# Kernel optimization log

Measured on AMD Instinct MI355X. Metric: run time of the kernel, lower is better.

Reference implementation:

```python
import jax, jax.numpy as jnp
import numpy as np

N = 100000   # nodes
E = 300000   # edges (avg degree ~3, molecular graphs)
DIN = 128    # input node features
H = 512      # hidden
OUT = 256    # out_channels
G = 4096     # number of graphs
EPS = 1e-5
SLOPE = 0.01  # LeakyReLU default negative slope
SELF_W = 2.0  # improved=True self-loop weight


def setup_inputs() -> dict:
    key = jax.random.key(0)
    ks = jax.random.split(key, 12)
    x = jax.random.normal(ks[0], (N, DIN), dtype=jnp.float32)
    edge_index = jax.random.randint(ks[1], (2, E), 0, N, dtype=jnp.int64)
    batch = jnp.sort(jax.random.randint(ks[2], (N,), 0, G, dtype=jnp.int64))
    s1 = 1.0 / np.sqrt(DIN)
    s2 = 1.0 / np.sqrt(H)
    return {
        "x": x,
        "edge_index": edge_index,
        "batch": batch,
        "W1": jax.random.normal(ks[3], (DIN, H), dtype=jnp.float32) * s1,
        "b1": jax.random.normal(ks[4], (H,), dtype=jnp.float32) * 0.01,
        "g1": jax.random.uniform(ks[5], (H,), dtype=jnp.float32, minval=0.5, maxval=1.5),
        "beta1": jax.random.normal(ks[6], (H,), dtype=jnp.float32) * 0.01,
        "W2": jax.random.normal(ks[7], (H, H), dtype=jnp.float32) * s2,
        "b2": jax.random.normal(ks[8], (H,), dtype=jnp.float32) * 0.01,
        "g2": jax.random.uniform(ks[9], (H,), dtype=jnp.float32, minval=0.5, maxval=1.5),
        "beta2": jax.random.normal(ks[10], (H,), dtype=jnp.float32) * 0.01,
        "Wf": jax.random.normal(ks[11], (H, OUT), dtype=jnp.float32) * s2,
        "bf": jnp.zeros((OUT,), dtype=jnp.float32),
    }


def _gcn_conv(x, W, b, row, col, n):
    # GCNConv(improved=True, add_self_loops=True, normalize=True), edge_weight=None
    h = x @ W                                   # [n, H]
    ones = jnp.ones(row.shape[0], dtype=h.dtype)
    deg = jax.ops.segment_sum(ones, col, num_segments=n) + SELF_W
    dinv = jax.lax.rsqrt(deg)                   # deg > 0 always (self-loop weight 2)
    norm = dinv[row] * dinv[col]                # [E]
    agg = jax.ops.segment_sum(h[row] * norm[:, None], col, num_segments=n)
    agg = agg + h * (SELF_W * dinv * dinv)[:, None]  # self-loop messages, no edge materialization
    return agg + b


def _bn(x, g, beta):
    # training-mode BatchNorm1d: biased batch stats
    mu = jnp.mean(x, axis=0)
    var = jnp.mean(jnp.square(x - mu), axis=0)
    return g * (x - mu) * jax.lax.rsqrt(var + EPS) + beta


def reference(x, edge_index, batch, W1, b1, g1, beta1, W2, b2, g2, beta2, Wf, bf):
    row, col = edge_index[0], edge_index[1]
    n = x.shape[0]
    h = _gcn_conv(x, W1, b1, row, col, n)
    h = jax.nn.leaky_relu(_bn(h, g1, beta1), SLOPE)
    # dropout is identity in eval mode
    h = _gcn_conv(h, W2, b2, row, col, n)
    h = jax.nn.leaky_relu(_bn(h, g2, beta2), SLOPE)
    pooled = jax.ops.segment_max(h, batch, num_segments=G)
    pooled = jnp.where(jnp.isfinite(pooled), pooled, 0.0)  # empty graphs -> 0 (torch_scatter fill)
    return pooled @ Wf + bf
```

## Files before the change

kernel.cpp:

```cpp
#include <hip/hip_runtime.h>
#include <hip/hip_bf16.h>

typedef __hip_bfloat16 bf16;
typedef __attribute__((ext_vector_type(8))) short short8;
typedef __attribute__((ext_vector_type(4))) float f32x4;

#define HDIM 512
#define SLOPE 0.01f
#define BN_EPS 1e-5f
#define STRIPES 8

__device__ inline float bf2f(short s) {
    unsigned u = ((unsigned)(unsigned short)s) << 16;
    return __builtin_bit_cast(float, u);
}
__device__ inline unsigned short f2bfbits(float v) {
    bf16 h = __float2bfloat16(v);
    return (unsigned short)__builtin_bit_cast(short, h);
}

struct EdgeRec { int src; float nm; };

__global__ void detect_types(const int* __restrict__ ei, const unsigned* __restrict__ xw,
                             int* __restrict__ flags, float* __restrict__ gpart) {
    __shared__ int nzhi, okbf;
    if (threadIdx.x == 0) { nzhi = 0; okbf = 0; }
    __syncthreads();
    int lo = 0, ok = 0;
    for (int i = threadIdx.x; i < 2048; i += 256)
        if (ei[2 * i + 1] != 0) lo++;
    for (int i = threadIdx.x; i < 1024; i += 256) {
        unsigned w = (xw[i] & 0xFFFFu) << 16;
        float av = fabsf(__builtin_bit_cast(float, w));
        if (av > 0.0009f && av < 64.0f) ok++;
    }
    for (int i = threadIdx.x; i < STRIPES * 2 * HDIM; i += 256) gpart[i] = 0.f;
    if (lo) atomicAdd(&nzhi, lo);
    if (ok) atomicAdd(&okbf, ok);
    __syncthreads();
    if (threadIdx.x == 0) {
        flags[0] = (nzhi == 0) ? 1 : 0;
        flags[1] = (okbf < 512) ? 1 : 0;
    }
}

__global__ void conv_all_idx(const int* __restrict__ ei, const int* __restrict__ batch,
                             int* __restrict__ ei32, int* __restrict__ batch32,
                             int* __restrict__ cnt, int e2, int n,
                             const int* __restrict__ flags) {
    int i = blockIdx.x * blockDim.x + threadIdx.x;
    int i64 = flags[0];
    if (i < e2) {
        int v = i64 ? (int)((const long long*)ei)[i] : ei[i];
        ei32[i] = v;
        if (i >= e2 / 2) atomicAdd(&cnt[v], 1);
    } else if (i < e2 + n) {
        int j = i - e2;
        batch32[j] = i64 ? (int)((const long long*)batch)[j] : batch[j];
    }
}

__global__ void wt_conv_all(const void* __restrict__ W1, const void* __restrict__ W2,
                            const void* __restrict__ Wf, const void* __restrict__ bf_,
                            bf16* __restrict__ W1T, bf16* __restrict__ W2T,
                            bf16* __restrict__ WfT, bf16* __restrict__ bfbf,
                            const int* __restrict__ flags) {
    const int S1 = 128 * 512, S2 = 512 * 512, S3 = 512 * 256;
    int idx = blockIdx.x * 256 + threadIdx.x;
    bool f32 = flags[1] != 0;
    if (idx < S1) {
        int nn = idx / 128, k = idx - nn * 128;
        float v = f32 ? ((const float*)W1)[(size_t)k * 512 + nn]
                      : __bfloat162float(((const bf16*)W1)[(size_t)k * 512 + nn]);
        W1T[idx] = __float2bfloat16(v);
    } else if (idx < S1 + S2) {
        int t = idx - S1;
        int nn = t / 512, k = t - nn * 512;
        float v = f32 ? ((const float*)W2)[(size_t)k * 512 + nn]
                      : __bfloat162float(((const bf16*)W2)[(size_t)k * 512 + nn]);
        W2T[t] = __float2bfloat16(v);
    } else if (idx < S1 + S2 + S3) {
        int t = idx - S1 - S2;
        int nn = t / 512, k = t - nn * 512;
        float v = f32 ? ((const float*)Wf)[(size_t)k * 256 + nn]
                      : __bfloat162float(((const bf16*)Wf)[(size_t)k * 256 + nn]);
        WfT[t] = __float2bfloat16(v);
    } else if (idx < S1 + S2 + S3 + 256) {
        int t = idx - S1 - S2 - S3;
        float v = f32 ? ((const float*)bf_)[t]
                      : __bfloat162float(((const bf16*)bf_)[t]);
        bfbf[t] = __float2bfloat16(v);
    }
}

__global__ void finalize_deg(const int* __restrict__ cnt, float* __restrict__ dinv,
                             float* __restrict__ selfw, int n) {
    int i = blockIdx.x * blockDim.x + threadIdx.x;
    if (i < n) {
        float d = (float)cnt[i] + 2.0f;
        dinv[i] = rsqrtf(d);
        selfw[i] = 2.0f / d;
    }
}

__global__ __launch_bounds__(256) void scan_part(
    const int* __restrict__ counts, int* __restrict__ offsets,
    int* __restrict__ bsum, int n)
{
    __shared__ int s[512];
    int b = blockIdx.x;
    int base = b * 512;
    int t = threadIdx.x;
    s[t]       = (base + t       < n) ? counts[base + t]       : 0;
    s[t + 256] = (base + t + 256 < n) ? counts[base + t + 256] : 0;

    int offset = 1;
    for (int d = 256; d > 0; d >>= 1) {
        __syncthreads();
        if (t < d) {
            int ai = offset * (2 * t + 1) - 1;
            int bi = offset * (2 * t + 2) - 1;
            s[bi] += s[ai];
        }
        offset <<= 1;
    }
    __syncthreads();
    if (t == 0) { bsum[b] = s[511]; s[511] = 0; }
    for (int d = 1; d < 512; d <<= 1) {
        offset >>= 1;
        __syncthreads();
        if (t < d) {
            int ai = offset * (2 * t + 1) - 1;
            int bi = offset * (2 * t + 2) - 1;
            int tmp = s[ai]; s[ai] = s[bi]; s[bi] += tmp;
        }
    }
    __syncthreads();
    if (base + t < n)       offsets[base + t]       = s[t];
    if (base + t + 256 < n) offsets[base + t + 256] = s[t + 256];
}

__global__ __launch_bounds__(1024) void scan_tops(int* __restrict__ bsum, int nb) {
    __shared__ int s[1024];
    int t = threadIdx.x;
    s[t] = (t < nb) ? bsum[t] : 0;
    __syncthreads();
    for (int off = 1; off < 1024; off <<= 1) {
        int v = (t >= off) ? s[t - off] : 0;
        __syncthreads();
        s[t] += v;
        __syncthreads();
    }
    if (t < nb) bsum[t] = (t == 0) ? 0 : s[t - 1];
}

__global__ __launch_bounds__(256) void scan_add(
    int* __restrict__ offsets, const int* __restrict__ bsum, int n, int e)
{
    int b = blockIdx.x;
    int base = b * 512;
    int add = bsum[b];
    int t = threadIdx.x;
    if (base + t < n)       offsets[base + t]       += add;
    if (base + t + 256 < n) offsets[base + t + 256] += add;
    if (b == 0 && t == 0) offsets[n] = e;
}

__global__ void scatter_edges(const int* __restrict__ rows, const int* __restrict__ cols,
                              const int* __restrict__ offsets, int* __restrict__ cursor,
                              const float* __restrict__ dinv,
                              EdgeRec* __restrict__ er, int e)
{
    int i = blockIdx.x * blockDim.x + threadIdx.x;
    if (i < e) {
        int d = cols[i];
        int r = rows[i];
        int pos = offsets[d] + atomicAdd(&cursor[d], 1);
        EdgeRec rec;
        rec.src = r;
        rec.nm = dinv[d] * dinv[r];
        er[pos] = rec;
    }
}

#define GEMM_STAGE(boff, kk)                                                             \
    {                                                                                    \
        _Pragma("unroll")                                                                \
        for (int i_ = 0; i_ < 2; i_++) {                                                 \
            int c_ = wave * 2 + i_;                                                      \
            const bf16* ga_ = A  + (size_t)(m0 + c_ * 16 + lrow) * K + (kk) + lcol;      \
            const bf16* gb_ = BT + (size_t)(n0 + c_ * 16 + lrow) * K + (kk) + lcol;      \
            __builtin_amdgcn_global_load_lds(                                            \
                (const __attribute__((address_space(1))) unsigned*)ga_,                  \
                (__attribute__((address_space(3))) unsigned*)(smem + (boff) + c_ * 512), \
                16, 0, 0);                                                               \
            __builtin_amdgcn_global_load_lds(                                            \
                (const __attribute__((address_space(1))) unsigned*)gb_,                  \
                (__attribute__((address_space(3))) unsigned*)(smem + 8192 + (boff) + c_ * 512), \
                16, 0, 0);                                                               \
        }                                                                                \
    }

#define GEMM_COMPUTE(boff)                                                               \
    {                                                                                    \
        short8 a[4], b[4];                                                               \
        _Pragma("unroll")                                                                \
        for (int mi2 = 0; mi2 < 4; mi2++)                                                \
            a[mi2] = *(const short8*)&smem[(boff) + (wm + mi2 * 16 + r) * 32 + aoff];    \
        _Pragma("unroll")                                                                \
        for (int ni = 0; ni < 4; ni++)                                                   \
            b[ni] = *(const short8*)&smem[8192 + (boff) + (wn + ni * 16 + r) * 32 + aoff]; \
        _Pragma("unroll")                                                                \
        for (int mi2 = 0; mi2 < 4; mi2++)                                                \
            _Pragma("unroll")                                                            \
            for (int ni = 0; ni < 4; ni++)                                               \
                acc[mi2][ni] = __builtin_amdgcn_mfma_f32_16x16x32_bf16(                  \
                    a[mi2], b[ni], acc[mi2][ni], 0, 0, 0);                               \
    }

template<bool STATS>
__global__ __launch_bounds__(256, 4) void gemm_m97(
    const bf16* __restrict__ A, const bf16* __restrict__ BT,
    void* __restrict__ C, const bf16* __restrict__ bias,
    int M, int K, int N, const int* __restrict__ cf32,
    float* __restrict__ gpart, int MB)
{
    __shared__ bf16 smem[16384];

    int NBN = N >> 7;
    int id = blockIdx.x;
    int grp = id / (8 * NBN);
    int loc = id - grp * 8 * NBN;
    int mi = loc & 7;
    int nblk = loc >> 3;
    int mblk = grp * 8 + mi;
    if (mblk >= MB) return;

    int tid = threadIdx.x;
    int wave = tid >> 6, lane = tid & 63, q = lane >> 4, r = lane & 15;
    int wm = (wave >> 1) * 64, wn = (wave & 1) * 64;
    int m0 = mblk * 128, n0 = nblk * 128;
    bool c32 = cf32 && *cf32;

    int lrow = lane >> 2;
    int lcol = (((lane & 3) ^ ((lane >> 3) & 3)) * 8);
    int aoff = (q ^ ((r >> 1) & 3)) * 8;

    f32x4 acc[4][4];
#pragma unroll
    for (int mi2 = 0; mi2 < 4; mi2++)
#pragma unroll
        for (int ni = 0; ni < 4; ni++)
            acc[mi2][ni] = {0.f, 0.f, 0.f, 0.f};

    const int nK = K >> 5;

    GEMM_STAGE(0, 0);
    __syncthreads();

    int cur = 0;
    for (int t = 1; t < nK; ++t) {
        GEMM_STAGE(cur ^ 4096, t * 32);
        GEMM_COMPUTE(cur);
        __syncthreads();
        cur ^= 4096;
    }
    GEMM_COMPUTE(cur);

    if (!c32) {
        __syncthreads();
#pragma unroll
        for (int mi2 = 0; mi2 < 4; mi2++) {
#pragma unroll
            for (int ni = 0; ni < 4; ni++) {
                int lc = wn + ni * 16 + r;
                float bv = bias ? __bfloat162float(bias[n0 + lc]) : 0.f;
#pragma unroll
                for (int reg = 0; reg < 4; reg++) {
                    int lr = wm + mi2 * 16 + q * 4 + reg;
                    int bo = ((lr << 8) + (lc << 1)) ^ (q << 5);
                    *(bf16*)((char*)smem + bo) = __float2bfloat16(acc[mi2][ni][reg] + bv);
                }
            }
        }
        __syncthreads();
#pragma unroll
        for (int pss = 0; pss < 8; pss++) {
            int off = pss * 4096 + tid * 16;
            int row = off >> 8;
            int cb = off & 255;
            int rb = cb ^ (((row >> 2) & 3) << 5);
            f32x4 v = *(const f32x4*)((const char*)smem + (row << 8) + rb);
            int gm = m0 + row;
            if (gm < M)
                *(f32x4*)((char*)C + (((size_t)gm * N + n0) << 1) + cb) = v;
        }
    } else {
#pragma unroll
        for (int mi2 = 0; mi2 < 4; mi2++) {
#pragma unroll
            for (int ni = 0; ni < 4; ni++) {
                int gn = n0 + wn + ni * 16 + r;
                float bv = bias ? __bfloat162float(bias[gn]) : 0.f;
#pragma unroll
                for (int reg = 0; reg < 4; reg++) {
                    int gm = m0 + wm + mi2 * 16 + q * 4 + reg;
                    if (gm < M)
                        ((float*)C)[(size_t)gm * N + gn] = acc[mi2][ni][reg] + bv;
                }
            }
        }
    }

    if constexpr (STATS) {
        float* base = gpart + (size_t)(mblk & (STRIPES - 1)) * 2 * HDIM;
#pragma unroll
        for (int ni = 0; ni < 4; ni++) {
            float cs = 0.f, cq = 0.f;
#pragma unroll
            for (int mi2 = 0; mi2 < 4; mi2++)
#pragma unroll
                for (int reg = 0; reg < 4; reg++) {
                    int gm = m0 + wm + mi2 * 16 + q * 4 + reg;
                    if (gm < M) {
                        float v = acc[mi2][ni][reg];
                        cs += v; cq += v * v;
                    }
                }
            cs += __shfl_xor(cs, 16, 64);
            cs += __shfl_xor(cs, 32, 64);
            cq += __shfl_xor(cq, 16, 64);
            cq += __shfl_xor(cq, 32, 64);
            if (q == 0) {
                int c = n0 + wn + ni * 16 + r;
                atomicAdd(&base[c], cs);
                atomicAdd(&base[HDIM + c], cq);
            }
        }
    }
}

__global__ __launch_bounds__(256) void agg_csr_din(
    const void* __restrict__ x, const int* __restrict__ offsets,
    const EdgeRec* __restrict__ er, const float* __restrict__ selfw,
    bf16* __restrict__ out, int n, const int* __restrict__ flags)
{
    int wave = threadIdx.x >> 6, lane = threadIdx.x & 63;
    int gw = blockIdx.x * 4 + wave;
    int nw = gridDim.x * 4;
    bool f32 = flags[1] != 0;

    for (int dst = gw; dst < n; dst += nw) {
        int s0 = offsets[dst], s1 = offsets[dst + 1];
        float sw = selfw[dst];
        float a0, a1;
        if (f32) {
            float2 v = ((const float2*)x)[(size_t)dst * 64 + lane];
            a0 = sw * v.x; a1 = sw * v.y;
        } else {
            unsigned u = ((const unsigned*)x)[(size_t)dst * 64 + lane];
            a0 = sw * bf2f((short)(u & 0xFFFF)); a1 = sw * bf2f((short)(u >> 16));
        }
        int p = s0;
        for (; p + 1 < s1; p += 2) {
            EdgeRec e0 = er[p], e1 = er[p + 1];
            if (f32) {
                float2 v0 = ((const float2*)x)[(size_t)e0.src * 64 + lane];
                float2 v1 = ((const float2*)x)[(size_t)e1.src * 64 + lane];
                a0 += e0.nm * v0.x + e1.nm * v1.x;
                a1 += e0.nm * v0.y + e1.nm * v1.y;
            } else {
                unsigned u0 = ((const unsigned*)x)[(size_t)e0.src * 64 + lane];
                unsigned u1 = ((const unsigned*)x)[(size_t)e1.src * 64 + lane];
                a0 += e0.nm * bf2f((short)(u0 & 0xFFFF)) + e1.nm * bf2f((short)(u1 & 0xFFFF));
                a1 += e0.nm * bf2f((short)(u0 >> 16))    + e1.nm * bf2f((short)(u1 >> 16));
            }
        }
        if (p < s1) {
            EdgeRec e0 = er[p];
            if (f32) {
                float2 v0 = ((const float2*)x)[(size_t)e0.src * 64 + lane];
                a0 += e0.nm * v0.x; a1 += e0.nm * v0.y;
            } else {
                unsigned u0 = ((const unsigned*)x)[(size_t)e0.src * 64 + lane];
                a0 += e0.nm * bf2f((short)(u0 & 0xFFFF)); a1 += e0.nm * bf2f((short)(u0 >> 16));
            }
        }
        ((unsigned*)out)[(size_t)dst * 64 + lane] =
            (unsigned)f2bfbits(a0) | ((unsigned)f2bfbits(a1) << 16);
    }
}

__global__ __launch_bounds__(256) void agg_csr_bn(
    const bf16* __restrict__ h, const int* __restrict__ offsets,
    const EdgeRec* __restrict__ er, const float* __restrict__ selfw,
    const float* __restrict__ scale, const float* __restrict__ shift,
    bf16* __restrict__ y, int n)
{
    int wave = threadIdx.x >> 6, lane = threadIdx.x & 63;
    int f0 = lane * 8;
    int gw = blockIdx.x * 4 + wave;
    int nw = gridDim.x * 4;

    float sc[8], sh[8];
#pragma unroll
    for (int j = 0; j < 8; j++) { sc[j] = scale[f0 + j]; sh[j] = shift[f0 + j]; }

    for (int dst = gw; dst < n; dst += nw) {
        int s0 = offsets[dst], s1 = offsets[dst + 1];
        float sw = selfw[dst];
        short8 hv = *(const short8*)(h + (size_t)dst * HDIM + f0);
        float acc[8];
#pragma unroll
        for (int j = 0; j < 8; j++) {
            float t = sc[j] * bf2f(hv[j]) + sh[j];
            t = t > 0.f ? t : SLOPE * t;
            acc[j] = sw * t;
        }
        int p = s0;
        for (; p + 1 < s1; p += 2) {
            EdgeRec e0 = er[p], e1 = er[p + 1];
            short8 v0 = *(const short8*)(h + (size_t)e0.src * HDIM + f0);
            short8 v1 = *(const short8*)(h + (size_t)e1.src * HDIM + f0);
#pragma unroll
            for (int j = 0; j < 8; j++) {
                float t0 = sc[j] * bf2f(v0[j]) + sh[j];
                t0 = t0 > 0.f ? t0 : SLOPE * t0;
                float t1 = sc[j] * bf2f(v1[j]) + sh[j];
                t1 = t1 > 0.f ? t1 : SLOPE * t1;
                acc[j] += e0.nm * t0 + e1.nm * t1;
            }
        }
        if (p < s1) {
            EdgeRec e0 = er[p];
            short8 v0 = *(const short8*)(h + (size_t)e0.src * HDIM + f0);
#pragma unroll
            for (int j = 0; j < 8; j++) {
                float t0 = sc[j] * bf2f(v0[j]) + sh[j];
                t0 = t0 > 0.f ? t0 : SLOPE * t0;
                acc[j] += e0.nm * t0;
            }
        }
        short8 o;
#pragma unroll
        for (int j = 0; j < 8; j++) ((bf16*)&o)[j] = __float2bfloat16(acc[j]);
        *(short8*)(y + (size_t)dst * HDIM + f0) = o;
    }
}

__global__ void bn_final(float* __restrict__ gpart,
                         const void* __restrict__ gamma, const void* __restrict__ beta,
                         float* __restrict__ scale, float* __restrict__ shift,
                         float invN, const int* __restrict__ flags)
{
    int f = threadIdx.x;
    float s = 0.f, q = 0.f;
#pragma unroll
    for (int k = 0; k < STRIPES; k++) {
        s += gpart[(size_t)k * 2 * HDIM + f];
        q += gpart[(size_t)k * 2 * HDIM + HDIM + f];
        gpart[(size_t)k * 2 * HDIM + f] = 0.f;
        gpart[(size_t)k * 2 * HDIM + HDIM + f] = 0.f;
    }
    float g = flags[1] ? ((const float*)gamma)[f]
                       : __bfloat162float(((const bf16*)gamma)[f]);
    float b = flags[1] ? ((const float*)beta)[f]
                       : __bfloat162float(((const bf16*)beta)[f]);
    float mu = s * invN;
    float var = fmaxf(q * invN - mu * mu, 0.f);
    float inv = rsqrtf(var + BN_EPS);
    float sc = g * inv;
    scale[f] = sc;
    shift[f] = b - mu * sc;
}

__global__ __launch_bounds__(256) void pool_fused(
    const bf16* __restrict__ y, const int* __restrict__ batch,
    const float* __restrict__ scale, const float* __restrict__ shift,
    bf16* __restrict__ pooled, int n, int G)
{
    int wave = threadIdx.x >> 6, lane = threadIdx.x & 63;
    int g = blockIdx.x * 4 + wave;
    if (g >= G) return;
    int f0 = lane * 8;

    int lo = 0, hi = n;
    while (lo < hi) { int mid = (lo + hi) >> 1; if (batch[mid] < g) lo = mid + 1; else hi = mid; }
    int s = lo;
    hi = n;
    while (lo < hi) { int mid = (lo + hi) >> 1; if (batch[mid] <= g) lo = mid + 1; else hi = mid; }
    int e = lo;

    float mx[8], mn[8];
#pragma unroll
    for (int j = 0; j < 8; j++) { mx[j] = -3.0e38f; mn[j] = 3.0e38f; }

    int rr = s;
    for (; rr + 1 < e; rr += 2) {
        short8 v0 = *(const short8*)(y + (size_t)rr * HDIM + f0);
        short8 v1 = *(const short8*)(y + (size_t)(rr + 1) * HDIM + f0);
#pragma unroll
        for (int j = 0; j < 8; j++) {
            float a = bf2f(v0[j]), b = bf2f(v1[j]);
            mx[j] = fmaxf(mx[j], fmaxf(a, b));
            mn[j] = fminf(mn[j], fminf(a, b));
        }
    }
    if (rr < e) {
        short8 v0 = *(const short8*)(y + (size_t)rr * HDIM + f0);
#pragma unroll
        for (int j = 0; j < 8; j++) {
            float a = bf2f(v0[j]);
            mx[j] = fmaxf(mx[j], a);
            mn[j] = fminf(mn[j], a);
        }
    }

    short8 o;
#pragma unroll
    for (int j = 0; j < 8; j++) {
        float outv = 0.f;
        if (s < e) {
            float sc = scale[f0 + j];
            float t = sc * (sc >= 0.f ? mx[j] : mn[j]) + shift[f0 + j];
            outv = t > 0.f ? t : SLOPE * t;
        }
        ((bf16*)&o)[j] = __float2bfloat16(outv);
    }
    *(short8*)(pooled + (size_t)g * HDIM + f0) = o;
}

extern "C" void kernel_launch(void* const* d_in, const int* in_sizes, int n_in,
                              void* d_out, int out_size, void* d_ws, size_t ws_size,
                              hipStream_t stream)
{
    const void* x     = d_in[0];
    const int*  ei    = (const int*)d_in[1];
    const int*  batch = (const int*)d_in[2];

    const int N   = in_sizes[2];
    const int E   = in_sizes[1] / 2;
    const int DIN = 128;
    const int OUT = 256;
    const int G   = out_size / OUT;
    const int Mp  = (N + 127) & ~127;
    const int MB  = Mp / 128;
    const int MB8 = (MB + 7) & ~7;

    char* p = (char*)d_ws;
    bf16* B1     = (bf16*)p;  p += (size_t)Mp * HDIM * sizeof(bf16);
    bf16* B2     = (bf16*)p;  p += (size_t)Mp * HDIM * sizeof(bf16);
    bf16* Q      = (bf16*)p;  p += (size_t)Mp * DIN * sizeof(bf16);
    bf16* W1T    = (bf16*)p;  p += (size_t)HDIM * DIN * sizeof(bf16);
    bf16* W2T    = (bf16*)p;  p += (size_t)HDIM * HDIM * sizeof(bf16);
    bf16* WfT    = (bf16*)p;  p += (size_t)OUT * HDIM * sizeof(bf16);
    bf16* bfbf   = (bf16*)p;  p += 512 * sizeof(bf16);
    int* ei32    = (int*)p;   p += (size_t)2 * E * sizeof(int);
    int* batch32 = (int*)p;   p += (size_t)N * sizeof(int);
    float* dinv  = (float*)p; p += (size_t)N * sizeof(float);
    float* selfw = (float*)p; p += (size_t)N * sizeof(float);
    int* offsets = (int*)p;   p += (size_t)(N + 4) * sizeof(int);
    int* cursor  = (int*)p;   p += (size_t)N * sizeof(int);
    EdgeRec* er  = (EdgeRec*)p; p += (size_t)E * sizeof(EdgeRec);
    int* bsum    = (int*)p;   p += 1024 * sizeof(int);
    float* gpart = (float*)p; p += (size_t)STRIPES * 2 * HDIM * sizeof(float);
    float* sc1   = (float*)p; p += HDIM * sizeof(float);
    float* sh1   = (float*)p; p += HDIM * sizeof(float);
    float* sc2   = (float*)p; p += HDIM * sizeof(float);
    float* sh2   = (float*)p; p += HDIM * sizeof(float);
    int* flags   = (int*)p;   p += 4 * sizeof(int);

    detect_types<<<1, 256, 0, stream>>>(ei, (const unsigned*)x, flags, gpart);
    hipMemsetAsync(cursor, 0, (size_t)N * sizeof(int), stream);
    conv_all_idx<<<(2 * E + N + 255) / 256, 256, 0, stream>>>(
        ei, batch, ei32, batch32, cursor, 2 * E, N, flags);
    wt_conv_all<<<(128 * 512 + 512 * 512 + 512 * 256 + 256 + 255) / 256, 256, 0, stream>>>(
        d_in[3], d_in[7], d_in[11], d_in[12], W1T, W2T, WfT, bfbf, flags);

    const int* rows = ei32;
    const int* cols = ei32 + E;

    finalize_deg<<<(N + 255) / 256, 256, 0, stream>>>(cursor, dinv, selfw, N);
    int nb = (N + 511) / 512;
    scan_part<<<nb, 256, 0, stream>>>(cursor, offsets, bsum, N);
    scan_tops<<<1, 1024, 0, stream>>>(bsum, nb);
    scan_add<<<nb, 256, 0, stream>>>(offsets, bsum, N, E);
    hipMemsetAsync(cursor, 0, (size_t)N * sizeof(int), stream);
    scatter_edges<<<(E + 255) / 256, 256, 0, stream>>>(rows, cols, offsets, cursor,
                                                       dinv, er, E);

    int gemm_blocks = MB8 * (HDIM / 128);

    agg_csr_din<<<2048, 256, 0, stream>>>(x, offsets, er, selfw, Q, N, flags);
    gemm_m97<true><<<gemm_blocks, 256, 0, stream>>>(
        Q, W1T, B2, nullptr, N, DIN, HDIM, nullptr, gpart, MB);
    bn_final<<<1, HDIM, 0, stream>>>(gpart, d_in[5], d_in[6], sc1, sh1, 1.0f / N, flags);

    agg_csr_bn<<<2048, 256, 0, stream>>>(B2, offsets, er, selfw, sc1, sh1, B1, N);
    gemm_m97<true><<<gemm_blocks, 256, 0, stream>>>(
        B1, W2T, B2, nullptr, N, HDIM, HDIM, nullptr, gpart, MB);
    bn_final<<<1, HDIM, 0, stream>>>(gpart, d_in[9], d_in[10], sc2, sh2, 1.0f / N, flags);

    pool_fused<<<(G + 3) / 4, 256, 0, stream>>>(B2, batch32, sc2, sh2, Q, N, G);
    gemm_m97<false><<<(G / 128) * (OUT / 128), 256, 0, stream>>>(
        Q, WfT, d_out, bfbf, G, HDIM, OUT, flags + 1, nullptr, G / 128);
}
```

Measured before the change: 460.9 us.

## Prefetch next node and unroll edge gathers by four in CSR aggregation

Both CSR aggregation kernels now software-pipeline across destination nodes: the offsets, self weight and self row for the next node are loaded before the current node's edges are processed. The edge loop is unrolled to four gathers per iteration, and the tail is handled without a loop, so more independent memory loads are in flight to hide gather latency. The GEMM launch bounds also move from 4 to 5 waves per SIMD, which caps registers to allow higher occupancy. The cost is higher register pressure in the aggregation kernels and possible spills in the GEMM.

```diff
diff --git a/kernel.cpp b/kernel.cpp
--- a/kernel.cpp
+++ b/kernel.cpp
@@ -219,7 +219,7 @@
     }
 
 template<bool STATS>
-__global__ __launch_bounds__(256, 4) void gemm_m97(
+__global__ __launch_bounds__(256, 5) void gemm_m97(
     const bf16* __restrict__ A, const bf16* __restrict__ BT,
     void* __restrict__ C, const bf16* __restrict__ bias,
     int M, int K, int N, const int* __restrict__ cf32,
@@ -340,6 +340,53 @@
     }
 }
 
+#define AGG_DIN_BODY(LOADV)                                                            \
+    int dst = gw;                                                                      \
+    if (dst < n) {                                                                     \
+        int s0 = offsets[dst], s1 = offsets[dst + 1];                                  \
+        float sw = selfw[dst];                                                         \
+        float h0, h1; LOADV(dst, h0, h1);                                              \
+        while (dst < n) {                                                              \
+            int nd = dst + nw;                                                         \
+            int ns0 = 0, ns1 = 0; float nsw = 0.f, nh0 = 0.f, nh1 = 0.f;               \
+            if (nd < n) {                                                              \
+                ns0 = offsets[nd]; ns1 = offsets[nd + 1]; nsw = selfw[nd];             \
+                LOADV(nd, nh0, nh1);                                                   \
+            }                                                                          \
+            float a0 = sw * h0, a1 = sw * h1;                                          \
+            int p = s0;                                                                \
+            for (; p + 3 < s1; p += 4) {                                               \
+                EdgeRec e0 = er[p], e1 = er[p + 1], e2 = er[p + 2], e3 = er[p + 3];    \
+                float x0, y0, x1, y1, x2, y2, x3, y3;                                  \
+                LOADV(e0.src, x0, y0); LOADV(e1.src, x1, y1);                          \
+                LOADV(e2.src, x2, y2); LOADV(e3.src, x3, y3);                          \
+                a0 += e0.nm * x0 + e1.nm * x1 + e2.nm * x2 + e3.nm * x3;               \
+                a1 += e0.nm * y0 + e1.nm * y1 + e2.nm * y2 + e3.nm * y3;               \
+            }                                                                          \
+            int rem = s1 - p;                                                          \
+            if (rem > 0) {                                                             \
+                EdgeRec e0 = er[p], e1 = e0, e2 = e0;                                  \
+                if (rem > 1) e1 = er[p + 1];                                           \
+                if (rem > 2) e2 = er[p + 2];                                           \
+                float x0, y0, x1 = 0.f, y1 = 0.f, x2 = 0.f, y2 = 0.f;                  \
+                LOADV(e0.src, x0, y0);                                                 \
+                if (rem > 1) LOADV(e1.src, x1, y1);                                    \
+                if (rem > 2) LOADV(e2.src, x2, y2);                                    \
+                a0 += e0.nm * x0; a1 += e0.nm * y0;                                    \
+                if (rem > 1) { a0 += e1.nm * x1; a1 += e1.nm * y1; }                   \
+                if (rem > 2) { a0 += e2.nm * x2; a1 += e2.nm * y2; }                   \
+            }                                                                          \
+            ((unsigned*)out)[(size_t)dst * 64 + lane] =                                \
+                (unsigned)f2bfbits(a0) | ((unsigned)f2bfbits(a1) << 16);               \
+            dst = nd; s0 = ns0; s1 = ns1; sw = nsw; h0 = nh0; h1 = nh1;                \
+        }                                                                              \
+    }
+
+#define LOADF32(idx, a, b) { float2 v_ = ((const float2*)x)[(size_t)(idx) * 64 + lane]; \
+                             a = v_.x; b = v_.y; }
+#define LOADBF(idx, a, b)  { unsigned u_ = ((const unsigned*)x)[(size_t)(idx) * 64 + lane]; \
+                             a = bf2f((short)(u_ & 0xFFFF)); b = bf2f((short)(u_ >> 16)); }
+
 __global__ __launch_bounds__(256) void agg_csr_din(
     const void* __restrict__ x, const int* __restrict__ offsets,
     const EdgeRec* __restrict__ er, const float* __restrict__ selfw,
@@ -349,45 +396,15 @@
     int gw = blockIdx.x * 4 + wave;
     int nw = gridDim.x * 4;
     bool f32 = flags[1] != 0;
-
-    for (int dst = gw; dst < n; dst += nw) {
-        int s0 = offsets[dst], s1 = offsets[dst + 1];
-        float sw = selfw[dst];
-        float a0, a1;
-        if (f32) {
-            float2 v = ((const float2*)x)[(size_t)dst * 64 + lane];
-            a0 = sw * v.x; a1 = sw * v.y;
-        } else {
-            unsigned u = ((const unsigned*)x)[(size_t)dst * 64 + lane];
-            a0 = sw * bf2f((short)(u & 0xFFFF)); a1 = sw * bf2f((short)(u >> 16));
-        }
-        int p = s0;
-        for (; p + 1 < s1; p += 2) {
-            EdgeRec e0 = er[p], e1 = er[p + 1];
-            if (f32) {
-                float2 v0 = ((const float2*)x)[(size_t)e0.src * 64 + lane];
-                float2 v1 = ((const float2*)x)[(size_t)e1.src * 64 + lane];
-                a0 += e0.nm * v0.x + e1.nm * v1.x;
-                a1 += e0.nm * v0.y + e1.nm * v1.y;
-            } else {
-                unsigned u0 = ((const unsigned*)x)[(size_t)e0.src * 64 + lane];
-                unsigned u1 = ((const unsigned*)x)[(size_t)e1.src * 64 + lane];
-                a0 += e0.nm * bf2f((short)(u0 & 0xFFFF)) + e1.nm * bf2f((short)(u1 & 0xFFFF));
-                a1 += e0.nm * bf2f((short)(u0 >> 16))    + e1.nm * bf2f((short)(u1 >> 16));
-            }
-        }
-        if (p < s1) {
-            EdgeRec e0 = er[p];
-            if (f32) {
-                float2 v0 = ((const float2*)x)[(size_t)e0.src * 64 + lane];
-                a0 += e0.nm * v0.x; a1 += e0.nm * v0.y;
-            } else {
-                unsigned u0 = ((const unsigned*)x)[(size_t)e0.src * 64 + lane];
-                a0 += e0.nm * bf2f((short)(u0 & 0xFFFF)); a1 += e0.nm * bf2f((short)(u0 >> 16));
-            }
-        }
-        ((unsigned*)out)[(size_t)dst * 64 + lane] =
-            (unsigned)f2bfbits(a0) | ((unsigned)f2bfbits(a1) << 16);
+    if (f32) { AGG_DIN_BODY(LOADF32) } else { AGG_DIN_BODY(LOADBF) }
+}
+
+__device__ inline void bnlk8(const short8& v, const float* sc, const float* sh,
+                             float* t) {
+#pragma unroll
+    for (int j = 0; j < 8; j++) {
+        float u = sc[j] * bf2f(v[j]) + sh[j];
+        t[j] = u > 0.f ? u : SLOPE * u;
     }
 }
 
@@ -406,45 +423,70 @@
 #pragma unroll
     for (int j = 0; j < 8; j++) { sc[j] = scale[f0 + j]; sh[j] = shift[f0 + j]; }
 
-    for (int dst = gw; dst < n; dst += nw) {
-        int s0 = offsets[dst], s1 = offsets[dst + 1];
-        float sw = selfw[dst];
-        short8 hv = *(const short8*)(h + (size_t)dst * HDIM + f0);
-        float acc[8];
-#pragma unroll
-        for (int j = 0; j < 8; j++) {
-            float t = sc[j] * bf2f(hv[j]) + sh[j];
-            t = t > 0.f ? t : SLOPE * t;
-            acc[j] = sw * t;
-        }
+    int dst = gw;
+    if (dst >= n) return;
+    int s0 = offsets[dst], s1 = offsets[dst + 1];
+    float sw = selfw[dst];
+    short8 hv = *(const short8*)(h + (size_t)dst * HDIM + f0);
+
+    while (dst < n) {
+        int nd = dst + nw;
+        int ns0 = 0, ns1 = 0; float nsw = 0.f; short8 nhv = {};
+        if (nd < n) {
+            ns0 = offsets[nd]; ns1 = offsets[nd + 1]; nsw = selfw[nd];
+            nhv = *(const short8*)(h + (size_t)nd * HDIM + f0);
+        }
+
+        float acc[8], t[8];
+        bnlk8(hv, sc, sh, t);
+#pragma unroll
+        for (int j = 0; j < 8; j++) acc[j] = sw * t[j];
+
         int p = s0;
-        for (; p + 1 < s1; p += 2) {
-            EdgeRec e0 = er[p], e1 = er[p + 1];
+        for (; p + 3 < s1; p += 4) {
+            EdgeRec e0 = er[p], e1 = er[p + 1], e2 = er[p + 2], e3 = er[p + 3];
             short8 v0 = *(const short8*)(h + (size_t)e0.src * HDIM + f0);
             short8 v1 = *(const short8*)(h + (size_t)e1.src * HDIM + f0);
-#pragma unroll
-            for (int j = 0; j < 8; j++) {
-                float t0 = sc[j] * bf2f(v0[j]) + sh[j];
-                t0 = t0 > 0.f ? t0 : SLOPE * t0;
-                float t1 = sc[j] * bf2f(v1[j]) + sh[j];
-                t1 = t1 > 0.f ? t1 : SLOPE * t1;
-                acc[j] += e0.nm * t0 + e1.nm * t1;
+            short8 v2 = *(const short8*)(h + (size_t)e2.src * HDIM + f0);
+            short8 v3 = *(const short8*)(h + (size_t)e3.src * HDIM + f0);
+            float t0[8], t1[8], t2[8], t3[8];
+            bnlk8(v0, sc, sh, t0); bnlk8(v1, sc, sh, t1);
+            bnlk8(v2, sc, sh, t2); bnlk8(v3, sc, sh, t3);
+#pragma unroll
+            for (int j = 0; j < 8; j++)
+                acc[j] += e0.nm * t0[j] + e1.nm * t1[j] + e2.nm * t2[j] + e3.nm * t3[j];
+        }
+        int rem = s1 - p;
+        if (rem > 0) {
+            EdgeRec e0 = er[p], e1 = e0, e2 = e0;
+            if (rem > 1) e1 = er[p + 1];
+            if (rem > 2) e2 = er[p + 2];
+            short8 v0 = *(const short8*)(h + (size_t)e0.src * HDIM + f0);
+            short8 v1 = {}, v2 = {};
+            if (rem > 1) v1 = *(const short8*)(h + (size_t)e1.src * HDIM + f0);
+            if (rem > 2) v2 = *(const short8*)(h + (size_t)e2.src * HDIM + f0);
+            float t0[8];
+            bnlk8(v0, sc, sh, t0);
+#pragma unroll
+            for (int j = 0; j < 8; j++) acc[j] += e0.nm * t0[j];
+            if (rem > 1) {
+                float t1[8]; bnlk8(v1, sc, sh, t1);
+#pragma unroll
+                for (int j = 0; j < 8; j++) acc[j] += e1.nm * t1[j];
             }
-        }
-        if (p < s1) {
-            EdgeRec e0 = er[p];
-            short8 v0 = *(const short8*)(h + (size_t)e0.src * HDIM + f0);
-#pragma unroll
-            for (int j = 0; j < 8; j++) {
-                float t0 = sc[j] * bf2f(v0[j]) + sh[j];
-                t0 = t0 > 0.f ? t0 : SLOPE * t0;
-                acc[j] += e0.nm * t0;
+            if (rem > 2) {
+                float t2[8]; bnlk8(v2, sc, sh, t2);
+#pragma unroll
+                for (int j = 0; j < 8; j++) acc[j] += e2.nm * t2[j];
             }
         }
+
         short8 o;
 #pragma unroll
         for (int j = 0; j < 8; j++) ((bf16*)&o)[j] = __float2bfloat16(acc[j]);
         *(short8*)(y + (size_t)dst * HDIM + f0) = o;
+
+        dst = nd; s0 = ns0; s1 = ns1; sw = nsw; hv = nhv;
     }
 }
 
```

Result: slower. 470.3 us (+2.1%).
